# Kernel tuning notes

Hardware: AMD Instinct MI355X
Metric: run time of the kernel (lower is better)

The kernel has to match this reference:

```python
import jax, jax.numpy as jnp
import numpy as np

ALPHA = 0.2  # LeakyReLU negative slope
NEG_INF = -9e15

def setup_inputs() -> dict:
    key = jax.random.key(0)
    k1, k2, k3, k4, k5 = jax.random.split(key, 5)
    B, N, Fin, Fout = 8, 2048, 128, 128
    h = jax.random.normal(k1, (B, N, Fin), dtype=jnp.float32)
    adj = jax.random.randint(k2, (N, N), 0, 2, dtype=jnp.int32)
    dist = jax.random.uniform(k3, (N, N), dtype=jnp.float32)
    W = jax.random.normal(k4, (Fin, Fout), dtype=jnp.float32) * (1.414 * (6.0 / (Fin + Fout)) ** 0.5)
    a = jax.random.normal(k5, (2 * Fout, 1), dtype=jnp.float32) * 0.1
    distance_scaler = jnp.ones((1,), dtype=jnp.float32)
    return {"h": h, "adj": adj, "dist": dist, "W": W, "a": a, "distance_scaler": distance_scaler}

def reference(h, adj, dist, W, a, distance_scaler):
    # h: [B,N,Fin], adj/dist: [N,N], W: [Fin,Fout], a: [2*Fout,1]
    h_prime = jnp.einsum('bnf,fh->bnh', h, W)              # [B,N,Fout]
    Fout = h_prime.shape[-1]
    a1, a2 = a[:Fout, 0], a[Fout:, 0]
    # additive score: a1.h_i + a2.h_j, equivalent to cat([h_i,h_j]) @ a
    si = h_prime @ a1                                      # [B,N]
    sj = h_prime @ a2                                      # [B,N]
    e = jax.nn.leaky_relu(si[:, :, None] + sj[:, None, :], negative_slope=ALPHA)  # [B,N,N]
    dist_bias = -jnp.log(dist + 1e-6) * distance_scaler[0]  # [N,N]
    scores = e + dist_bias[None, :, :]
    scores = jnp.where(adj[None, :, :] > 0, scores, NEG_INF)
    attention = jax.nn.softmax(scores, axis=2)             # [B,N,N]
    # dropout=identity in eval mode
    out = jnp.einsum('bij,bjh->bih', attention, h_prime)   # [B,N,Fout]
    return jax.nn.elu(out)
```

## Files before the change

kernel.cpp:

```cpp
#include <hip/hip_runtime.h>
#include <hip/hip_bf16.h>

typedef __attribute__((ext_vector_type(4))) float f32x4;
typedef __attribute__((ext_vector_type(8))) short short8;
typedef __attribute__((ext_vector_type(4))) unsigned short ushort4v;
typedef _Float16 f16x8 __attribute__((ext_vector_type(8)));

#define NB 8
#define NN 2048
#define NF 128
#define LOG2E 1.4426950408889634f
#define MASK_NEG_H -60000.0f

static __device__ __forceinline__ unsigned short f2bf(float f) {
    union { __hip_bfloat16 b; unsigned short u; } cv;
    cv.b = __float2bfloat16(f);
    return cv.u;
}

__global__ __launch_bounds__(256) void k_pre(
    const float* __restrict__ h, const int* __restrict__ adj,
    const float* __restrict__ dist, const float* __restrict__ W,
    const float* __restrict__ a, const float* __restrict__ scaler,
    unsigned short* __restrict__ vfrag, float* __restrict__ siC,
    float* __restrict__ sjC, _Float16* __restrict__ biasF)
{
    __shared__ __align__(16) unsigned char smem[34816];
    const int bid = blockIdx.x;
    const int t = threadIdx.x;

    if (bid < 256) {
        unsigned char* WT = smem;
        float* wa1 = (float*)(smem + 32768);
        float* wa2 = wa1 + NF;

        const int lane = t & 63;
        const int w = t >> 6;
        const int b = bid >> 5;
        const int i0 = (bid & 31) << 6;

        {
            const int f = t >> 1;
            const int c0 = (t & 1) << 6;
            float s1 = 0.f, s2 = 0.f;
            const float* wrow = W + f * NF + c0;
            const float* a1p = a + c0;
            const float* a2p = a + NF + c0;
            #pragma unroll 8
            for (int c = 0; c < 64; ++c) {
                float wv = wrow[c];
                s1 += wv * a1p[c];
                s2 += wv * a2p[c];
                int col = c0 + c;
                int dst = col * 256 + ((2 * f) ^ ((col & 15) << 4));
                *reinterpret_cast<unsigned short*>(&WT[dst]) = f2bf(wv);
            }
            s1 += __shfl_xor(s1, 1);
            s2 += __shfl_xor(s2, 1);
            if ((t & 1) == 0) { wa1[f] = s1 * LOG2E; wa2[f] = s2 * LOG2E; }
        }
        __syncthreads();

        const int l15 = lane & 15;
        const int arow = i0 + w * 16 + l15;
        const int kofs = (lane >> 4) << 3;
        const float* hrow = h + (size_t)(b * NN + arow) * NF + kofs;
        const int swz = l15 << 4;

        f32x4 acc[8];
        #pragma unroll
        for (int nt = 0; nt < 8; ++nt) acc[nt] = (f32x4)(0.f);
        float s1 = 0.f, s2 = 0.f;

        #pragma unroll
        for (int k0 = 0; k0 < NF; k0 += 32) {
            f32x4 h0 = *reinterpret_cast<const f32x4*>(hrow + k0);
            f32x4 h1 = *reinterpret_cast<const f32x4*>(hrow + k0 + 4);
            f32x4 w1lo = *reinterpret_cast<const f32x4*>(&wa1[k0 + kofs]);
            f32x4 w1hi = *reinterpret_cast<const f32x4*>(&wa1[k0 + kofs + 4]);
            f32x4 w2lo = *reinterpret_cast<const f32x4*>(&wa2[k0 + kofs]);
            f32x4 w2hi = *reinterpret_cast<const f32x4*>(&wa2[k0 + kofs + 4]);
            short8 af;
            #pragma unroll
            for (int e = 0; e < 4; ++e) {
                s1 += h0[e] * w1lo[e] + h1[e] * w1hi[e];
                s2 += h0[e] * w2lo[e] + h1[e] * w2hi[e];
                af[e]     = (short)f2bf(h0[e]);
                af[4 + e] = (short)f2bf(h1[e]);
            }
            const int ib = (2 * (k0 + kofs)) ^ swz;
            #pragma unroll
            for (int nt = 0; nt < 8; ++nt) {
                short8 bf8 = *reinterpret_cast<short8*>(&WT[(nt * 16 + l15) * 256 + ib]);
                acc[nt] = __builtin_amdgcn_mfma_f32_16x16x32_bf16(af, bf8, acc[nt], 0, 0, 0);
            }
        }

        s1 += __shfl_xor(s1, 16); s1 += __shfl_xor(s1, 32);
        s2 += __shfl_xor(s2, 16); s2 += __shfl_xor(s2, 32);
        if (lane < 16) {
            siC[b * NN + arow] = s1;
            sjC[b * NN + arow] = s2;
        }

        const int J0 = i0 + w * 16 + ((lane >> 4) << 2);
        const int s = J0 >> 5;
        const int jq = (J0 >> 3) & 3;
        const int eh = J0 & 7;
        #pragma unroll
        for (int nt = 0; nt < 8; ++nt) {
            ushort4v pk;
            #pragma unroll
            for (int e = 0; e < 4; ++e) pk[e] = f2bf(acc[nt][e]);
            *reinterpret_cast<ushort4v*>(
                vfrag + (((size_t)(b * 64 + s) * 8 + nt) * 64 + (l15 | (jq << 4))) * 8 + eh) = pk;
        }
    } else {
        _Float16 (*st)[64][8] = (_Float16 (*)[64][8])smem;
        const int bid2 = bid - 256;
        const int iblk = bid2 >> 3;
        const int jch = bid2 & 7;
        const int i_l = t >> 4;
        const int o2 = t & 15;
        const int i = iblk * 16 + i_l;
        const int jbase = jch * 256 + o2 * 16;
        const float sc = scaler[0];

        const int* ap = adj + (size_t)i * NN + jbase;
        const float* dp = dist + (size_t)i * NN + jbase;
        int av[16]; float dv[16];
        *reinterpret_cast<int4*>(&av[0])  = *reinterpret_cast<const int4*>(ap);
        *reinterpret_cast<int4*>(&av[4])  = *reinterpret_cast<const int4*>(ap + 4);
        *reinterpret_cast<int4*>(&av[8])  = *reinterpret_cast<const int4*>(ap + 8);
        *reinterpret_cast<int4*>(&av[12]) = *reinterpret_cast<const int4*>(ap + 12);
        *reinterpret_cast<float4*>(&dv[0])  = *reinterpret_cast<const float4*>(dp);
        *reinterpret_cast<float4*>(&dv[4])  = *reinterpret_cast<const float4*>(dp + 4);
        *reinterpret_cast<float4*>(&dv[8])  = *reinterpret_cast<const float4*>(dp + 8);
        *reinterpret_cast<float4*>(&dv[12]) = *reinterpret_cast<const float4*>(dp + 12);

        #pragma unroll
        for (int u = 0; u < 2; ++u) {
            const int sl = (o2 * 2 + u) >> 2;
            const int jq = (o2 * 2 + u) & 3;
            f16x8 pk;
            #pragma unroll
            for (int e = 0; e < 8; ++e) {
                const int idx = u * 8 + e;
                float v = (av[idx] > 0) ? (-__log2f(dv[idx] + 1e-6f) * sc) : MASK_NEG_H;
                pk[e] = (_Float16)v;
            }
            *reinterpret_cast<f16x8*>(&st[sl][i_l | (jq << 4)][0]) = pk;
        }
        __syncthreads();

        const int w = t >> 6, lane = t & 63;
        #pragma unroll
        for (int sub = 0; sub < 2; ++sub) {
            const int fs = w * 2 + sub;
            *reinterpret_cast<f16x8*>(
                biasF + ((size_t)(iblk * 64 + jch * 8 + fs) * 64 + lane) * 8) =
                *reinterpret_cast<f16x8*>(&st[fs][lane][0]);
        }
    }
}

__global__ __launch_bounds__(512, 4) void k_attn(
    const unsigned short* __restrict__ vfrag, const float* __restrict__ siC,
    const float* __restrict__ sjC, const _Float16* __restrict__ biasF,
    float* __restrict__ out)
{
    __shared__ __align__(16) float red[4][8][64][4];
    __shared__ float lp[2][4][16];

    const int t = threadIdx.x;
    const int lane = t & 63;
    const int w = t >> 6;
    const int rt = w & 3;
    const int jh = w >> 2;
    const int l15 = lane & 15;
    const int hi = lane >> 4;

    const int b = blockIdx.x & 7;
    const int rg = blockIdx.x >> 3;

    const int rowbase = rg * 64 + rt * 16;
    const float si0 = siC[b * NN + rowbase + l15];

    const float* sjp = sjC + b * NN + jh * 1024 + hi * 8;
    const _Float16* bp = biasF +
        ((size_t)((rg * 4 + rt) * 64 + jh * 32) * 64 + lane) * 8;
    const unsigned short* vp = vfrag +
        ((size_t)(b * 64 + jh * 32) * 8) * 512 + lane * 8;

    f32x4 acc[8];
    #pragma unroll
    for (int ct = 0; ct < 8; ++ct) acc[ct] = (f32x4)(0.f);
    float ls0 = 0.f;

    #pragma unroll 2
    for (int sl = 0; sl < 32; ++sl) {
        f32x4 sj0 = *reinterpret_cast<const f32x4*>(sjp + sl * 32);
        f32x4 sj1 = *reinterpret_cast<const f32x4*>(sjp + sl * 32 + 4);
        f16x8 bv = *reinterpret_cast<const f16x8*>(bp + sl * 512);
        short8 pa;
        #pragma unroll
        for (int e = 0; e < 8; ++e) {
            const float sjv = (e < 4) ? sj0[e] : sj1[e - 4];
            float x = si0 + sjv;
            x = fmaxf(x, 0.2f * x) + (float)bv[e];
            float p = __builtin_amdgcn_exp2f(x);
            ls0 += p;
            pa[e] = (short)f2bf(p);
        }
        const unsigned short* vs = vp + sl * 4096;
        #pragma unroll
        for (int ct = 0; ct < 8; ++ct) {
            const short8 bfr = *reinterpret_cast<const short8*>(vs + ct * 512);
            acc[ct] = __builtin_amdgcn_mfma_f32_16x16x32_bf16(pa, bfr, acc[ct], 0, 0, 0);
        }
    }

    ls0 += __shfl_xor(ls0, 16);
    ls0 += __shfl_xor(ls0, 32);
    if (lane < 16) lp[jh][rt][l15] = ls0;

    if (jh == 1) {
        #pragma unroll
        for (int ct = 0; ct < 8; ++ct)
            *reinterpret_cast<f32x4*>(&red[rt][ct][lane][0]) = acc[ct];
    }
    __syncthreads();
    if (jh == 0) {
        float linv[4];
        #pragma unroll
        for (int e = 0; e < 4; ++e) {
            const int rr = (hi << 2) + e;
            linv[e] = 1.0f / (lp[0][rt][rr] + lp[1][rt][rr]);
        }
        #pragma unroll
        for (int ct = 0; ct < 8; ++ct) {
            f32x4 o = acc[ct] + *reinterpret_cast<const f32x4*>(&red[rt][ct][lane][0]);
            const int col = ct * 16 + l15;
            #pragma unroll
            for (int e = 0; e < 4; ++e) {
                const int row = rowbase + (hi << 2) + e;
                float v = o[e] * linv[e];
                v = (v > 0.f) ? v : expm1f(v);
                out[(size_t)(b * NN + row) * NF + col] = v;
            }
        }
    }
}

extern "C" void kernel_launch(void* const* d_in, const int* in_sizes, int n_in,
                              void* d_out, int out_size, void* d_ws, size_t ws_size,
                              hipStream_t stream) {
    (void)in_sizes; (void)n_in; (void)out_size; (void)ws_size;
    const float* h      = (const float*)d_in[0];
    const int*   adj    = (const int*)d_in[1];
    const float* dist   = (const float*)d_in[2];
    const float* W      = (const float*)d_in[3];
    const float* a      = (const float*)d_in[4];
    const float* scaler = (const float*)d_in[5];
    float* out = (float*)d_out;

    char* ws = (char*)d_ws;
    unsigned short* vfrag = (unsigned short*)ws;
    float* siC      = (float*)(ws + 4 * 1024 * 1024);
    float* sjC      = (float*)(ws + 4 * 1024 * 1024 + 65536);
    _Float16* biasF = (_Float16*)(ws + 4 * 1024 * 1024 + 2 * 65536);

    k_pre<<<dim3(1280), dim3(256), 0, stream>>>(h, adj, dist, W, a, scaler,
                                                vfrag, siC, sjC, biasF);
    k_attn<<<dim3(NB * NN / 64), dim3(512), 0, stream>>>(vfrag, siC, sjC, biasF, out);
}
```

Before: 46.76 us.

## Stage V fragments through triple-buffered LDS with async global-to-LDS loads

The attention kernel now loads the value fragments cooperatively into a three-stage LDS ring using global_load_lds. All 8 waves share one copy per tile, where before each wave read its own fragments from global memory. Softmax score inputs (sj, bias) are prefetched a tile ahead, and the loop is synchronised with vmcnt waits and barriers. This cuts redundant global traffic for V and overlaps loads with MFMA work. The cost is 96KB of LDS, which lowers occupancy (launch bounds relaxed to match), plus two barriers per tile.

```diff
diff --git a/kernel.cpp b/kernel.cpp
--- a/kernel.cpp
+++ b/kernel.cpp
@@ -16,6 +16,12 @@
     union { __hip_bfloat16 b; unsigned short u; } cv;
     cv.b = __float2bfloat16(f);
     return cv.u;
+}
+
+static __device__ __forceinline__ void gload_lds16(const void* g, void* l) {
+    __builtin_amdgcn_global_load_lds(
+        (const __attribute__((address_space(1))) unsigned int*)g,
+        (__attribute__((address_space(3))) unsigned int*)l, 16, 0, 0);
 }
 
 __global__ __launch_bounds__(256) void k_pre(
@@ -164,12 +170,12 @@
     }
 }
 
-__global__ __launch_bounds__(512, 4) void k_attn(
+__global__ __launch_bounds__(512) void k_attn(
     const unsigned short* __restrict__ vfrag, const float* __restrict__ siC,
     const float* __restrict__ sjC, const _Float16* __restrict__ biasF,
     float* __restrict__ out)
 {
-    __shared__ __align__(16) float red[4][8][64][4];
+    __shared__ __align__(16) unsigned char vbuf[3][32768];
     __shared__ float lp[2][4][16];
 
     const int t = threadIdx.x;
@@ -186,48 +192,88 @@
     const int rowbase = rg * 64 + rt * 16;
     const float si0 = siC[b * NN + rowbase + l15];
 
-    const float* sjp = sjC + b * NN + jh * 1024 + hi * 8;
-    const _Float16* bp = biasF +
-        ((size_t)((rg * 4 + rt) * 64 + jh * 32) * 64 + lane) * 8;
-    const unsigned short* vp = vfrag +
-        ((size_t)(b * 64 + jh * 32) * 8) * 512 + lane * 8;
+    const unsigned short* vsrc = vfrag + (size_t)b * 262144 + w * 512 + lane * 8;
+    const int ldst = w * 1024;
+
+    const _Float16* bp = biasF + ((size_t)((rg * 4 + rt) * 64) * 64 + lane) * 8;
+    const float* sjb = sjC + b * NN + hi * 8;
 
     f32x4 acc[8];
     #pragma unroll
     for (int ct = 0; ct < 8; ++ct) acc[ct] = (f32x4)(0.f);
     float ls0 = 0.f;
 
-    #pragma unroll 2
-    for (int sl = 0; sl < 32; ++sl) {
-        f32x4 sj0 = *reinterpret_cast<const f32x4*>(sjp + sl * 32);
-        f32x4 sj1 = *reinterpret_cast<const f32x4*>(sjp + sl * 32 + 4);
-        f16x8 bv = *reinterpret_cast<const f16x8*>(bp + sl * 512);
-        short8 pa;
-        #pragma unroll
-        for (int e = 0; e < 8; ++e) {
-            const float sjv = (e < 4) ? sj0[e] : sj1[e - 4];
-            float x = si0 + sjv;
-            x = fmaxf(x, 0.2f * x) + (float)bv[e];
-            float p = __builtin_amdgcn_exp2f(x);
-            ls0 += p;
-            pa[e] = (short)f2bf(p);
-        }
-        const unsigned short* vs = vp + sl * 4096;
-        #pragma unroll
-        for (int ct = 0; ct < 8; ++ct) {
-            const short8 bfr = *reinterpret_cast<const short8*>(vs + ct * 512);
-            acc[ct] = __builtin_amdgcn_mfma_f32_16x16x32_bf16(pa, bfr, acc[ct], 0, 0, 0);
-        }
-    }
+#define STAGE(TL, BUF)                                                        \
+    { const unsigned short* gs = vsrc + (TL) * 16384;                         \
+      unsigned char* lb = &vbuf[BUF][ldst];                                   \
+      gload_lds16(gs,         lb);                                            \
+      gload_lds16(gs + 4096,  lb + 8192);                                     \
+      gload_lds16(gs + 8192,  lb + 16384);                                    \
+      gload_lds16(gs + 12288, lb + 24576); }
+
+    f32x4 sjA0, sjA1, sjB0, sjB1;
+    f16x8 bvA, bvB;
+
+#define PREFETCH_SB(TL)                                                       \
+    { const int sA = (TL) * 4 + jh * 2;                                       \
+      sjA0 = *reinterpret_cast<const f32x4*>(sjb + sA * 32);                  \
+      sjA1 = *reinterpret_cast<const f32x4*>(sjb + sA * 32 + 4);              \
+      bvA  = *reinterpret_cast<const f16x8*>(bp + sA * 512);                  \
+      sjB0 = *reinterpret_cast<const f32x4*>(sjb + sA * 32 + 32);             \
+      sjB1 = *reinterpret_cast<const f32x4*>(sjb + sA * 32 + 36);             \
+      bvB  = *reinterpret_cast<const f16x8*>(bp + sA * 512 + 512); }
+
+#define QSTEP(SJ0, SJ1, BV, LSL, BUF)                                         \
+    { short8 pa;                                                              \
+      _Pragma("unroll")                                                       \
+      for (int e = 0; e < 8; ++e) {                                           \
+          const float sjv = (e < 4) ? SJ0[e] : SJ1[e - 4];                    \
+          float x = si0 + sjv;                                                \
+          x = fmaxf(x, 0.2f * x) + (float)BV[e];                              \
+          float p = __builtin_amdgcn_exp2f(x);                                \
+          ls0 += p;                                                           \
+          pa[e] = (short)f2bf(p);                                             \
+      }                                                                       \
+      _Pragma("unroll")                                                       \
+      for (int ct = 0; ct < 8; ++ct) {                                        \
+          const short8 bfr = *reinterpret_cast<const short8*>(                \
+              &vbuf[BUF][((LSL) * 8 + ct) * 1024 + lane * 16]);               \
+          acc[ct] = __builtin_amdgcn_mfma_f32_16x16x32_bf16(pa, bfr, acc[ct], 0, 0, 0); \
+      } }
+
+    STAGE(0, 0)
+    PREFETCH_SB(0)
+    STAGE(1, 1)
+
+    for (int tl = 0; tl < 15; ++tl) {
+        const int buf = tl % 3;
+        asm volatile("s_waitcnt vmcnt(10)" ::: "memory");
+        __builtin_amdgcn_s_barrier();
+        QSTEP(sjA0, sjA1, bvA, jh * 2, buf)
+        QSTEP(sjB0, sjB1, bvB, jh * 2 + 1, buf)
+        PREFETCH_SB(tl + 1)
+        if (tl + 2 < 16) STAGE(tl + 2, (tl + 2) % 3)
+        __builtin_amdgcn_s_barrier();
+    }
+    {
+        asm volatile("s_waitcnt vmcnt(6)" ::: "memory");
+        __builtin_amdgcn_s_barrier();
+        QSTEP(sjA0, sjA1, bvA, jh * 2, 0)
+        QSTEP(sjB0, sjB1, bvB, jh * 2 + 1, 0)
+    }
+#undef STAGE
+#undef PREFETCH_SB
+#undef QSTEP
 
     ls0 += __shfl_xor(ls0, 16);
     ls0 += __shfl_xor(ls0, 32);
     if (lane < 16) lp[jh][rt][l15] = ls0;
+    __syncthreads();
 
     if (jh == 1) {
         #pragma unroll
         for (int ct = 0; ct < 8; ++ct)
-            *reinterpret_cast<f32x4*>(&red[rt][ct][lane][0]) = acc[ct];
+            *reinterpret_cast<f32x4*>(&vbuf[1][(rt * 8 + ct) * 1024 + lane * 16]) = acc[ct];
     }
     __syncthreads();
     if (jh == 0) {
@@ -239,7 +285,8 @@
         }
         #pragma unroll
         for (int ct = 0; ct < 8; ++ct) {
-            f32x4 o = acc[ct] + *reinterpret_cast<const f32x4*>(&red[rt][ct][lane][0]);
+            f32x4 o = acc[ct] + *reinterpret_cast<const f32x4*>(
+                &vbuf[1][(rt * 8 + ct) * 1024 + lane * 16]);
             const int col = ct * 16 + l15;
             #pragma unroll
             for (int e = 0; e < 4; ++e) {
```

Measured after the change: 43.45 us. 7.1% less time.
